# Kernel optimization log

Measured on AMD Instinct MI355X. Metric: run time of the kernel, lower is better.

The kernel has to match this reference:

```python
import jax, jax.numpy as jnp
import numpy as np

NUM_CLUSTERS = 256
NUM_HEADS = 16
DIM_PER_HEAD = 64
NGRAM_VOCAB = 768 * 256
NGRAM_EMB_DIM = 8
DECAY = 0.999
EPS_PQ = 1e-06
LN_EPS = 1e-05


def _first_primes_after(start, count):
    primes = []
    n = start
    while len(primes) < count:
        n += 1
        if all(n % p for p in range(2, int(n ** 0.5) + 1)):
            primes.append(n)
    return np.array(primes, dtype=np.int64)

# first NUM_HEADS primes in (NGRAM_VOCAB, 2*NGRAM_VOCAB), matching sympy.primerange
_PRIMES = _first_primes_after(NGRAM_VOCAB, NUM_HEADS)


def _layer_norm(v, scale, bias):
    # reduction over last axis; per-(head, feature) scale/bias (flax feature_axes=(-2,-1))
    mu = jnp.mean(v, axis=-1, keepdims=True)
    var = jnp.var(v, axis=-1, keepdims=True)
    return (v - mu) * jax.lax.rsqrt(var + LN_EPS) * scale + bias


def setup_inputs() -> dict:
    key = jax.random.key(0)
    k1, k2, k3 = jax.random.split(key, 3)
    B, L = 4, 4096
    x = jax.random.normal(k1, (B, L, NUM_HEADS * DIM_PER_HEAD), dtype=jnp.float32)
    means = jax.random.normal(k2, (NUM_HEADS, NUM_CLUSTERS, DIM_PER_HEAD), dtype=jnp.float32)
    embed_table = jax.random.normal(k3, (NGRAM_VOCAB * NUM_HEADS, NGRAM_EMB_DIM), dtype=jnp.float32)
    ln_x_scale = jnp.ones((NUM_HEADS, DIM_PER_HEAD), dtype=jnp.float32)
    ln_x_bias = jnp.zeros((NUM_HEADS, DIM_PER_HEAD), dtype=jnp.float32)
    ln_y_scale = jnp.ones((NUM_HEADS, NGRAM_EMB_DIM), dtype=jnp.float32)
    ln_y_bias = jnp.zeros((NUM_HEADS, NGRAM_EMB_DIM), dtype=jnp.float32)
    return {"x": x, "means": means, "embed_table": embed_table,
            "ln_x_scale": ln_x_scale, "ln_x_bias": ln_x_bias,
            "ln_y_scale": ln_y_scale, "ln_y_bias": ln_y_bias}


def reference(x, means, embed_table, ln_x_scale, ln_x_bias, ln_y_scale, ln_y_bias):
    B, L, HD = x.shape
    H, K, D = means.shape
    E = NGRAM_EMB_DIM
    xh = x.reshape(B, L, H, D)

    # --- ProductQuantization: squared-distance cluster assignment ---
    x_sq = jnp.sum(jnp.square(xh), axis=-1, keepdims=True)            # [B,L,H,1]
    m_sq = jnp.sum(jnp.square(means), axis=-1)[None, None]            # [1,1,H,K]
    dists = x_sq + m_sq - 2.0 * jnp.einsum('blhd,hkd->blhk', xh, means)
    cluster_ids = jnp.argmin(dists, axis=-1).astype(jnp.int32)        # [B,L,H]

    # --- EMA means update (train-mode side effect) ---
    one_hot = jax.nn.one_hot(cluster_ids, K, dtype=xh.dtype)          # [B,L,H,K]
    counts = jnp.sum(one_hot, axis=(0, 1))                            # [H,K]
    sum_x = jnp.einsum('blhk,blhd->hkd', one_hot, xh)                 # [H,K,D]
    means_x = sum_x / (EPS_PQ + counts[..., None])
    new_means = (1.0 - DECAY) * means_x + DECAY * means

    # --- bigram ids: ids[t] + ids[t-1] * vocab ---
    prev = jnp.pad(cluster_ids[:, :-1], ((0, 0), (1, 0), (0, 0)))     # [B,L,H]
    ngram_cluster_ids = cluster_ids + prev * NUM_CLUSTERS             # < K*K, fits int32

    # --- multi-way hash per head ---
    head = jnp.arange(H, dtype=jnp.int32)                             # [H]
    primes = jnp.asarray(_PRIMES, dtype=jnp.int32)                    # [H]
    hashed = (ngram_cluster_ids * (head + 1) + (head + 1)) % primes % NGRAM_VOCAB
    ngram_ids = hashed + NGRAM_VOCAB * head                           # [B,L,H]

    # --- ngram embedding gather + per-head LayerNorms + concat ---
    y = embed_table[ngram_ids]                                        # [B,L,H,E]
    normed_x = _layer_norm(xh, ln_x_scale, ln_x_bias)
    normed_y = _layer_norm(y, ln_y_scale, ln_y_bias)
    out = jnp.concatenate((normed_x[..., : D - E], normed_y), axis=-1)
    out = out.reshape(B, L, H * D)
    return out, new_means
```

## Files before the change

### kernel.cpp

```cpp
#include <hip/hip_runtime.h>
#include <cstdint>
#include <cstddef>

#define NH 16
#define ND 64
#define NK 256
#define NE 8
#define NV 196608
#define NBL 16384
#define TOK 64
#define ACC_STRIDE 257

struct Primes { int p[NH]; };

__global__ __launch_bounds__(256, 2) void k_pq(
    const float* __restrict__ x, const float* __restrict__ means,
    const float* __restrict__ lnxs, const float* __restrict__ lnxb,
    float* __restrict__ out, uint8_t* __restrict__ cids,
    float* __restrict__ gsum, int* __restrict__ gcnt)
{
  __shared__ __align__(16) float smem[16704];
  float4* sx4   = (float4*)smem;
  float4* sm4   = (float4*)(smem + 4096);
  float*  smsq  = smem + 12288;
  float*  lnsc  = smem + 12544;
  float*  lnbi  = smem + 12608;
  float*  accum = smem;
  int*    scnt  = (int*)(smem + 16448);

  const int tid     = threadIdx.x;
  const int h       = blockIdx.y;
  const int g0      = blockIdx.x * TOK;
  const int tok_row = tid >> 4;
  const int cl_col  = tid & 15;

  {
    const int t = tid >> 2, part = tid & 3;
    const float4* xs = (const float4*)(x + ((size_t)(g0 + t) * NH + h) * ND) + part * 4;
#pragma unroll
    for (int j = 0; j < 4; ++j) sx4[(part * 4 + j) * TOK + t] = xs[j];
  }
  if (tid < ND) { lnsc[tid] = lnxs[h * ND + tid]; lnbi[tid] = lnxb[h * ND + tid]; }
  scnt[tid] = 0;

  float acc[4][16];
#pragma unroll
  for (int j = 0; j < 4; ++j)
#pragma unroll
    for (int i = 0; i < 16; ++i) acc[j][i] = 0.f;

  for (int half = 0; half < 2; ++half) {
    if (half) __syncthreads();
    {
      const float4* msrc = (const float4*)(means + ((size_t)h * NK + tid) * ND + half * 32);
      float mp = 0.f;
#pragma unroll
      for (int i = 0; i < 8; ++i) {
        float4 v = msrc[i];
        sm4[i * NK + tid] = v;
        mp += v.x * v.x + v.y * v.y + v.z * v.z + v.w * v.w;
      }
      if (half == 0) smsq[tid] = mp; else smsq[tid] += mp;
    }
    __syncthreads();

#pragma unroll 2
    for (int dc = 0; dc < 8; ++dc) {
      float4 xv[4];
#pragma unroll
      for (int j = 0; j < 4; ++j) xv[j] = sx4[(half * 8 + dc) * TOK + tok_row * 4 + j];
#pragma unroll
      for (int i = 0; i < 16; ++i) {
        float4 mv = sm4[dc * NK + i * 16 + cl_col];
#pragma unroll
        for (int j = 0; j < 4; ++j) {
          float a = acc[j][i];
          a = fmaf(xv[j].x, mv.x, a);
          a = fmaf(xv[j].y, mv.y, a);
          a = fmaf(xv[j].z, mv.z, a);
          a = fmaf(xv[j].w, mv.w, a);
          acc[j][i] = a;
        }
      }
    }
  }

  int bk[4];
  {
    float bv[4]; int bi[4];
#pragma unroll
    for (int j = 0; j < 4; ++j) { bv[j] = 3.4e38f; bi[j] = 0; }
#pragma unroll
    for (int i = 0; i < 16; ++i) {
      const int c = i * 16 + cl_col;
      const float mq = smsq[c];
#pragma unroll
      for (int j = 0; j < 4; ++j) {
        float d = mq - 2.0f * acc[j][i];
        if (d < bv[j]) { bv[j] = d; bi[j] = c; }
      }
    }
#pragma unroll
    for (int j = 0; j < 4; ++j) {
      float v = bv[j]; int c = bi[j];
#pragma unroll
      for (int m = 1; m < 16; m <<= 1) {
        float ov = __shfl_xor(v, m);
        int   oc = __shfl_xor(c, m);
        if (ov < v || (ov == v && oc < c)) { v = ov; c = oc; }
      }
      bk[j] = c;
    }
    if (cl_col == 0) {
#pragma unroll
      for (int j = 0; j < 4; ++j) {
        const int t = tok_row * 4 + j;
        cids[(size_t)(g0 + t) * NH + h] = (uint8_t)bk[j];
        atomicAdd(&scnt[bk[j]], 1);
      }
    }
  }

  {
    const int t = tid >> 2, q = tid & 3;
    float4 v[4];
    float s = 0.f, sq = 0.f;
#pragma unroll
    for (int j = 0; j < 4; ++j) {
      v[j] = sx4[(q * 4 + j) * TOK + t];
      s  += v[j].x + v[j].y + v[j].z + v[j].w;
      sq += v[j].x * v[j].x + v[j].y * v[j].y + v[j].z * v[j].z + v[j].w * v[j].w;
    }
    s  += __shfl_xor(s, 1);  sq += __shfl_xor(sq, 1);
    s  += __shfl_xor(s, 2);  sq += __shfl_xor(sq, 2);
    float mu  = s * (1.f / 64.f);
    float var = sq * (1.f / 64.f) - mu * mu;
    float rs  = rsqrtf(var + 1e-5f);
    float* orow = out + ((size_t)(g0 + t) * NH + h) * ND;
#pragma unroll
    for (int j = 0; j < 4; ++j) {
      const int dc = q * 4 + j;
      if (dc < 14) {
        float4 o;
        o.x = (v[j].x - mu) * rs * lnsc[dc * 4 + 0] + lnbi[dc * 4 + 0];
        o.y = (v[j].y - mu) * rs * lnsc[dc * 4 + 1] + lnbi[dc * 4 + 1];
        o.z = (v[j].z - mu) * rs * lnsc[dc * 4 + 2] + lnbi[dc * 4 + 2];
        o.w = (v[j].w - mu) * rs * lnsc[dc * 4 + 3] + lnbi[dc * 4 + 3];
        ((float4*)orow)[dc] = o;
      }
    }
  }

  float4 xr[4];
#pragma unroll
  for (int j = 0; j < 4; ++j) xr[j] = sx4[cl_col * TOK + tok_row * 4 + j];

  __syncthreads();
  for (int idx = tid; idx < 64 * ACC_STRIDE; idx += 256) accum[idx] = 0.f;
  __syncthreads();

#pragma unroll
  for (int j = 0; j < 4; ++j) {
    const int b = bk[j];
    atomicAdd(&accum[(cl_col * 4 + 0) * ACC_STRIDE + b], xr[j].x);
    atomicAdd(&accum[(cl_col * 4 + 1) * ACC_STRIDE + b], xr[j].y);
    atomicAdd(&accum[(cl_col * 4 + 2) * ACC_STRIDE + b], xr[j].z);
    atomicAdd(&accum[(cl_col * 4 + 3) * ACC_STRIDE + b], xr[j].w);
  }
  __syncthreads();

  const int cnt = scnt[tid];
  if (cnt > 0) atomicAdd(&gcnt[h * NK + tid], cnt);
  const bool act = cnt > 0;
#pragma unroll 4
  for (int d = 0; d < ND; ++d) {
    if (act) atomicAdd(&gsum[((size_t)h * ND + d) * NK + tid], accum[d * ACC_STRIDE + tid]);
  }
}

__global__ __launch_bounds__(256) void k_ngram(
    const uint8_t* __restrict__ cids, const float* __restrict__ embed,
    const float* __restrict__ lys, const float* __restrict__ lyb,
    float* __restrict__ out, Primes pr)
{
  const int i = blockIdx.x * 256 + threadIdx.x;
  const int h = i & 15;
  const int g = i >> 4;
  const int l = g & 4095;

  int cid  = (int)cids[i];
  int prev = (l == 0) ? 0 : (int)cids[i - NH];
  int ng   = cid + (prev << 8);
  int hp1  = h + 1;
  int v    = ng * hp1 + hp1;
  const int p = pr.p[h];
  while (v >= p) v -= p;
  if (v >= NV) v -= NV;

  const float4* e4 = (const float4*)(embed + ((size_t)(v + NV * h)) * NE);
  float4 y0 = e4[0], y1 = e4[1];

  float s = ((y0.x + y0.y) + (y0.z + y0.w)) + ((y1.x + y1.y) + (y1.z + y1.w));
  float mu = s * 0.125f;
  float q = y0.x * y0.x + y0.y * y0.y + y0.z * y0.z + y0.w * y0.w
          + y1.x * y1.x + y1.y * y1.y + y1.z * y1.z + y1.w * y1.w;
  float var = q * 0.125f - mu * mu;
  float rs  = rsqrtf(var + 1e-5f);

  const float* sc = lys + h * NE;
  const float* bi = lyb + h * NE;
  float4 o0, o1;
  o0.x = (y0.x - mu) * rs * sc[0] + bi[0];
  o0.y = (y0.y - mu) * rs * sc[1] + bi[1];
  o0.z = (y0.z - mu) * rs * sc[2] + bi[2];
  o0.w = (y0.w - mu) * rs * sc[3] + bi[3];
  o1.x = (y1.x - mu) * rs * sc[4] + bi[4];
  o1.y = (y1.y - mu) * rs * sc[5] + bi[5];
  o1.z = (y1.z - mu) * rs * sc[6] + bi[6];
  o1.w = (y1.w - mu) * rs * sc[7] + bi[7];

  float4* orow = (float4*)(out + ((size_t)g * NH + h) * ND + 56);
  orow[0] = o0;
  orow[1] = o1;
}

__global__ __launch_bounds__(256) void k_means(
    const float* __restrict__ means, const float* __restrict__ gsum,
    const int* __restrict__ gcnt, float* __restrict__ newm)
{
  const int i = blockIdx.x * 256 + threadIdx.x;
  const int d = i & 63;
  const int k = (i >> 6) & 255;
  const int h = i >> 14;
  float cnt = (float)gcnt[h * NK + k];
  float sx  = gsum[((size_t)h * ND + d) * NK + k];
  float mx  = sx / (1e-6f + cnt);
  newm[i] = 0.001f * mx + 0.999f * means[i];
}

extern "C" void kernel_launch(void* const* d_in, const int* in_sizes, int n_in,
                              void* d_out, int out_size, void* d_ws, size_t ws_size,
                              hipStream_t stream)
{
  const float* x     = (const float*)d_in[0];
  const float* means = (const float*)d_in[1];
  const float* embed = (const float*)d_in[2];
  const float* lnxs  = (const float*)d_in[3];
  const float* lnxb  = (const float*)d_in[4];
  const float* lys   = (const float*)d_in[5];
  const float* lyb   = (const float*)d_in[6];

  float* out  = (float*)d_out;
  float* newm = out + (size_t)NBL * NH * ND;

  float*   gsum = (float*)d_ws;
  int*     gcnt = (int*)((char*)d_ws + (size_t)NH * NK * ND * 4);
  uint8_t* cids = (uint8_t*)((char*)d_ws + (size_t)NH * NK * ND * 4 + (size_t)NH * NK * 4);

  hipMemsetAsync(d_ws, 0, (size_t)NH * NK * ND * 4 + (size_t)NH * NK * 4, stream);

  Primes pr;
  {
    int n = NV, c = 0;
    while (c < NH) {
      ++n;
      bool isp = true;
      for (int q = 2; (long long)q * q <= n; ++q)
        if (n % q == 0) { isp = false; break; }
      if (isp) pr.p[c++] = n;
    }
  }

  dim3 g1(NBL / TOK, NH);
  k_pq<<<g1, 256, 0, stream>>>(x, means, lnxs, lnxb, out, cids, gsum, gcnt);
  k_ngram<<<(NBL * NH) / 256, 256, 0, stream>>>(cids, embed, lys, lyb, out, pr);
  k_means<<<(NH * NK * ND) / 256, 256, 0, stream>>>(means, gsum, gcnt, newm);
}
```

Before: 339.7 us.

## Restructure PQ kernel to 512 threads with padded means tile and direct x loads

The cluster-assignment kernel moves from 256 to 512 threads per block. It now stages the full 64-dim means tile once, padded to avoid bank conflicts, instead of in two halves, and reads x directly from global memory rather than through shared memory. Each thread now handles 8 clusters for 4 tokens, and the argmin reduction spans a full 32-lane group. The LayerNorm and scatter-accumulate phases re-read x from global, and the global atomic flush is split across both halves of the block. This cuts per-thread register use and removes a barrier-separated means reload, at the cost of redundant global/L2 reads of x and larger shared memory per block, which may limit occupancy.

Result: no change. 336.7 us (-0.9%).

```diff
diff --git a/kernel.cpp b/kernel.cpp
--- a/kernel.cpp
+++ b/kernel.cpp
@@ -9,172 +9,156 @@
 #define NV 196608
 #define NBL 16384
 #define TOK 64
+#define MROW 17
 #define ACC_STRIDE 257
 
 struct Primes { int p[NH]; };
 
-__global__ __launch_bounds__(256, 2) void k_pq(
+__global__ __launch_bounds__(512, 4) void k_pq(
     const float* __restrict__ x, const float* __restrict__ means,
     const float* __restrict__ lnxs, const float* __restrict__ lnxb,
     float* __restrict__ out, uint8_t* __restrict__ cids,
     float* __restrict__ gsum, int* __restrict__ gcnt)
 {
-  __shared__ __align__(16) float smem[16704];
-  float4* sx4   = (float4*)smem;
-  float4* sm4   = (float4*)(smem + 4096);
-  float*  smsq  = smem + 12288;
-  float*  lnsc  = smem + 12544;
-  float*  lnbi  = smem + 12608;
+  __shared__ __align__(16) float smem[18176];
+  float4* sm4   = (float4*)smem;
+  float*  smsq2 = smem + 17408;
+  int*    scnt  = (int*)(smem + 17920);
   float*  accum = smem;
-  int*    scnt  = (int*)(smem + 16448);
-
-  const int tid     = threadIdx.x;
-  const int h       = blockIdx.y;
-  const int g0      = blockIdx.x * TOK;
-  const int tok_row = tid >> 4;
-  const int cl_col  = tid & 15;
-
-  {
-    const int t = tid >> 2, part = tid & 3;
-    const float4* xs = (const float4*)(x + ((size_t)(g0 + t) * NH + h) * ND) + part * 4;
-#pragma unroll
-    for (int j = 0; j < 4; ++j) sx4[(part * 4 + j) * TOK + t] = xs[j];
-  }
-  if (tid < ND) { lnsc[tid] = lnxs[h * ND + tid]; lnbi[tid] = lnxb[h * ND + tid]; }
-  scnt[tid] = 0;
-
-  float acc[4][16];
+
+  const int tid = threadIdx.x;
+  const int c   = tid & 31;
+  const int r   = tid >> 5;
+  const int h   = blockIdx.y;
+  const int g0  = blockIdx.x * TOK;
+
+  {
+    const int cl = tid & 255, hf = tid >> 8;
+    const float4* src = (const float4*)(means + ((size_t)h * NK + cl) * ND + hf * 32);
+    float mp = 0.f;
+#pragma unroll
+    for (int i = 0; i < 8; ++i) {
+      float4 v = src[i];
+      sm4[cl * MROW + hf * 8 + i] = v;
+      mp += v.x * v.x + v.y * v.y + v.z * v.z + v.w * v.w;
+    }
+    smsq2[hf * NK + cl] = mp;
+    if (tid < NK) scnt[tid] = 0;
+  }
+  __syncthreads();
+
+  float acc[4][8];
 #pragma unroll
   for (int j = 0; j < 4; ++j)
 #pragma unroll
-    for (int i = 0; i < 16; ++i) acc[j][i] = 0.f;
-
-  for (int half = 0; half < 2; ++half) {
-    if (half) __syncthreads();
-    {
-      const float4* msrc = (const float4*)(means + ((size_t)h * NK + tid) * ND + half * 32);
-      float mp = 0.f;
-#pragma unroll
-      for (int i = 0; i < 8; ++i) {
-        float4 v = msrc[i];
-        sm4[i * NK + tid] = v;
-        mp += v.x * v.x + v.y * v.y + v.z * v.z + v.w * v.w;
-      }
-      if (half == 0) smsq[tid] = mp; else smsq[tid] += mp;
-    }
-    __syncthreads();
+    for (int i = 0; i < 8; ++i) acc[j][i] = 0.f;
+
+  const float* xb = x + ((size_t)(g0 + r * 4) * NH + h) * ND;
 
 #pragma unroll 2
-    for (int dc = 0; dc < 8; ++dc) {
-      float4 xv[4];
-#pragma unroll
-      for (int j = 0; j < 4; ++j) xv[j] = sx4[(half * 8 + dc) * TOK + tok_row * 4 + j];
-#pragma unroll
-      for (int i = 0; i < 16; ++i) {
-        float4 mv = sm4[dc * NK + i * 16 + cl_col];
-#pragma unroll
-        for (int j = 0; j < 4; ++j) {
-          float a = acc[j][i];
-          a = fmaf(xv[j].x, mv.x, a);
-          a = fmaf(xv[j].y, mv.y, a);
-          a = fmaf(xv[j].z, mv.z, a);
-          a = fmaf(xv[j].w, mv.w, a);
-          acc[j][i] = a;
-        }
+  for (int dc = 0; dc < 16; ++dc) {
+    float4 xv[4];
+#pragma unroll
+    for (int j = 0; j < 4; ++j)
+      xv[j] = *(const float4*)(xb + j * (NH * ND) + dc * 4);
+#pragma unroll
+    for (int i = 0; i < 8; ++i) {
+      float4 mv = sm4[(i * 32 + c) * MROW + dc];
+#pragma unroll
+      for (int j = 0; j < 4; ++j) {
+        float a = acc[j][i];
+        a = fmaf(xv[j].x, mv.x, a);
+        a = fmaf(xv[j].y, mv.y, a);
+        a = fmaf(xv[j].z, mv.z, a);
+        a = fmaf(xv[j].w, mv.w, a);
+        acc[j][i] = a;
       }
     }
   }
 
   int bk[4];
   {
-    float bv[4]; int bi[4];
-#pragma unroll
-    for (int j = 0; j < 4; ++j) { bv[j] = 3.4e38f; bi[j] = 0; }
-#pragma unroll
-    for (int i = 0; i < 16; ++i) {
-      const int c = i * 16 + cl_col;
-      const float mq = smsq[c];
+    float bv[4]; int bi_[4];
+#pragma unroll
+    for (int j = 0; j < 4; ++j) { bv[j] = 3.4e38f; bi_[j] = 0; }
+#pragma unroll
+    for (int i = 0; i < 8; ++i) {
+      const int cl = i * 32 + c;
+      const float mq = smsq2[cl] + smsq2[NK + cl];
 #pragma unroll
       for (int j = 0; j < 4; ++j) {
         float d = mq - 2.0f * acc[j][i];
-        if (d < bv[j]) { bv[j] = d; bi[j] = c; }
+        if (d < bv[j]) { bv[j] = d; bi_[j] = cl; }
       }
     }
 #pragma unroll
     for (int j = 0; j < 4; ++j) {
-      float v = bv[j]; int c = bi[j];
-#pragma unroll
-      for (int m = 1; m < 16; m <<= 1) {
+      float v = bv[j]; int id = bi_[j];
+#pragma unroll
+      for (int m = 1; m < 32; m <<= 1) {
         float ov = __shfl_xor(v, m);
-        int   oc = __shfl_xor(c, m);
-        if (ov < v || (ov == v && oc < c)) { v = ov; c = oc; }
-      }
-      bk[j] = c;
-    }
-    if (cl_col == 0) {
+        int   oi = __shfl_xor(id, m);
+        if (ov < v || (ov == v && oi < id)) { v = ov; id = oi; }
+      }
+      bk[j] = id;
+    }
+    if (c == 0) {
 #pragma unroll
       for (int j = 0; j < 4; ++j) {
-        const int t = tok_row * 4 + j;
-        cids[(size_t)(g0 + t) * NH + h] = (uint8_t)bk[j];
+        cids[(size_t)(g0 + r * 4 + j) * NH + h] = (uint8_t)bk[j];
         atomicAdd(&scnt[bk[j]], 1);
       }
     }
   }
 
-  {
-    const int t = tid >> 2, q = tid & 3;
-    float4 v[4];
-    float s = 0.f, sq = 0.f;
-#pragma unroll
-    for (int j = 0; j < 4; ++j) {
-      v[j] = sx4[(q * 4 + j) * TOK + t];
-      s  += v[j].x + v[j].y + v[j].z + v[j].w;
-      sq += v[j].x * v[j].x + v[j].y * v[j].y + v[j].z * v[j].z + v[j].w * v[j].w;
-    }
-    s  += __shfl_xor(s, 1);  sq += __shfl_xor(sq, 1);
-    s  += __shfl_xor(s, 2);  sq += __shfl_xor(sq, 2);
-    float mu  = s * (1.f / 64.f);
-    float var = sq * (1.f / 64.f) - mu * mu;
-    float rs  = rsqrtf(var + 1e-5f);
-    float* orow = out + ((size_t)(g0 + t) * NH + h) * ND;
-#pragma unroll
-    for (int j = 0; j < 4; ++j) {
-      const int dc = q * 4 + j;
-      if (dc < 14) {
+  __syncthreads();
+  for (int idx = tid; idx < ND * ACC_STRIDE; idx += 512) accum[idx] = 0.f;
+  __syncthreads();
+
+#pragma unroll
+  for (int j = 0; j < 4; ++j) {
+    const float* xt = x + ((size_t)(g0 + r * 4 + j) * NH + h) * ND + c * 2;
+    float2 v = *(const float2*)xt;
+    atomicAdd(&accum[(c * 2 + 0) * ACC_STRIDE + bk[j]], v.x);
+    atomicAdd(&accum[(c * 2 + 1) * ACC_STRIDE + bk[j]], v.y);
+  }
+
+  {
+    const int tl = tid >> 4, q = tid & 15;
+#pragma unroll
+    for (int rep = 0; rep < 2; ++rep) {
+      const int t = tl + rep * 32;
+      float4 v = *(const float4*)(x + ((size_t)(g0 + t) * NH + h) * ND + q * 4);
+      float s  = v.x + v.y + v.z + v.w;
+      float sq = v.x * v.x + v.y * v.y + v.z * v.z + v.w * v.w;
+#pragma unroll
+      for (int m = 1; m < 16; m <<= 1) { s += __shfl_xor(s, m); sq += __shfl_xor(sq, m); }
+      float mu  = s * (1.f / 64.f);
+      float var = sq * (1.f / 64.f) - mu * mu;
+      float rs  = rsqrtf(var + 1e-5f);
+      if (q < 14) {
+        float4 sc = *(const float4*)(lnxs + h * ND + q * 4);
+        float4 bi = *(const float4*)(lnxb + h * ND + q * 4);
         float4 o;
-        o.x = (v[j].x - mu) * rs * lnsc[dc * 4 + 0] + lnbi[dc * 4 + 0];
-        o.y = (v[j].y - mu) * rs * lnsc[dc * 4 + 1] + lnbi[dc * 4 + 1];
-        o.z = (v[j].z - mu) * rs * lnsc[dc * 4 + 2] + lnbi[dc * 4 + 2];
-        o.w = (v[j].w - mu) * rs * lnsc[dc * 4 + 3] + lnbi[dc * 4 + 3];
-        ((float4*)orow)[dc] = o;
-      }
-    }
-  }
-
-  float4 xr[4];
-#pragma unroll
-  for (int j = 0; j < 4; ++j) xr[j] = sx4[cl_col * TOK + tok_row * 4 + j];
-
-  __syncthreads();
-  for (int idx = tid; idx < 64 * ACC_STRIDE; idx += 256) accum[idx] = 0.f;
-  __syncthreads();
-
-#pragma unroll
-  for (int j = 0; j < 4; ++j) {
-    const int b = bk[j];
-    atomicAdd(&accum[(cl_col * 4 + 0) * ACC_STRIDE + b], xr[j].x);
-    atomicAdd(&accum[(cl_col * 4 + 1) * ACC_STRIDE + b], xr[j].y);
-    atomicAdd(&accum[(cl_col * 4 + 2) * ACC_STRIDE + b], xr[j].z);
-    atomicAdd(&accum[(cl_col * 4 + 3) * ACC_STRIDE + b], xr[j].w);
-  }
-  __syncthreads();
-
-  const int cnt = scnt[tid];
-  if (cnt > 0) atomicAdd(&gcnt[h * NK + tid], cnt);
-  const bool act = cnt > 0;
+        o.x = (v.x - mu) * rs * sc.x + bi.x;
+        o.y = (v.y - mu) * rs * sc.y + bi.y;
+        o.z = (v.z - mu) * rs * sc.z + bi.z;
+        o.w = (v.w - mu) * rs * sc.w + bi.w;
+        *(float4*)(out + ((size_t)(g0 + t) * NH + h) * ND + q * 4) = o;
+      }
+    }
+  }
+  __syncthreads();
+
+  {
+    const int cl = tid & 255, dh = tid >> 8;
+    const int cnt = scnt[cl];
+    if (cnt > 0) {
+      if (dh == 0) atomicAdd(&gcnt[h * NK + cl], cnt);
 #pragma unroll 4
-  for (int d = 0; d < ND; ++d) {
-    if (act) atomicAdd(&gsum[((size_t)h * ND + d) * NK + tid], accum[d * ACC_STRIDE + tid]);
+      for (int d = dh * 32; d < dh * 32 + 32; ++d)
+        atomicAdd(&gsum[((size_t)h * ND + d) * NK + cl], accum[d * ACC_STRIDE + cl]);
+    }
   }
 }
 
@@ -272,7 +256,7 @@
   }
 
   dim3 g1(NBL / TOK, NH);
-  k_pq<<<g1, 256, 0, stream>>>(x, means, lnxs, lnxb, out, cids, gsum, gcnt);
+  k_pq<<<g1, 512, 0, stream>>>(x, means, lnxs, lnxb, out, cids, gsum, gcnt);
   k_ngram<<<(NBL * NH) / 256, 256, 0, stream>>>(cids, embed, lys, lyb, out, pr);
   k_means<<<(NH * NK * ND) / 256, 256, 0, stream>>>(means, gsum, gcnt, newm);
 }
```
